# Kernel tuning notes

Measured on AMD Instinct MI355X. Metric: run time of the kernel, lower is better.

## Reference

```python
import jax, jax.numpy as jnp
import numpy as np

DIM = 192
STATE = 64
B = 8
H = 64
W = 64
EPS_LN = 1e-5
EPS_BN = 1e-5


def _layernorm(x, g, b):
    m = jnp.mean(x, axis=-1, keepdims=True)
    v = jnp.mean((x - m) ** 2, axis=-1, keepdims=True)
    return (x - m) / jnp.sqrt(v + EPS_LN) * g + b


def _linear(x, w, b=None):
    # torch Linear convention: w is [out, in]
    y = jnp.einsum('...i,oi->...o', x, w)
    return y if b is None else y + b


def _parallel_scan(A, Bd, xp):
    # A, Bd, xp: [B, L, S]; h_t = A_t*h_{t-1} + Bd_t*xp_t via log-space cumsum
    A_safe = jnp.clip(A, 0.001, 0.999)
    log_A = jnp.log(A_safe + 1e-10)
    log_cum_A = jnp.cumsum(log_A, axis=1)
    log_cum_A_max = jnp.max(log_cum_A, axis=1, keepdims=True)
    cum_A = jnp.exp(log_cum_A - log_cum_A_max)
    BX = Bd * xp
    # prepend zeros, drop last: normalizer uses cumprod up to t-1
    log_pad = jnp.pad(log_cum_A - log_cum_A_max, ((0, 0), (1, 0), (0, 0)))[:, :-1]
    BX_norm = BX * jnp.exp(-log_pad)
    return jnp.cumsum(BX_norm, axis=1) * cum_A


def _ssm(x, ln_g, ln_b, xp_w, xp_b, dt_w, dt_b, A_log, B_w, C_w, Dp, out_w, out_b):
    xn = _layernorm(x, ln_g, ln_b)
    delta = jax.nn.softplus(_linear(xn, dt_w, dt_b)) * 0.01 + 0.0001  # [B,L,S]
    B_t = _linear(xn, B_w)
    C_t = _linear(xn, C_w)
    A = -jnp.exp(A_log)  # [S]
    x_proj = _linear(xn, xp_w, xp_b)
    deltaA = jnp.clip(delta * A, -10.0, -0.0001)
    A_disc = jnp.exp(deltaA)
    B_disc = delta * B_t
    h = _parallel_scan(A_disc, B_disc, x_proj)
    y = C_t * h
    y = jnp.where(jnp.all(jnp.isfinite(y)), y, jnp.zeros_like(y))
    y = _linear(y, out_w, out_b)
    return y + jnp.clip(Dp, -2.0, 2.0) * x


def reference(x, ln1_g, ln1_b, ln2_g, ln2_b, dw_w, bn_g, bn_b, bn_rm, bn_rv,
              ssm_ln_g, ssm_ln_b, xp_w, xp_b, dt_w, dt_b, A_log, B_w, C_w,
              D_param, out_w, out_b, mlp_w1, mlp_b1, mlp_w2, mlp_b2,
              alpha_local, alpha_ssm, alpha_mlp):
    identity = x
    # depthwise 3x3 conv + BatchNorm2d (eval mode, running stats)
    xc = jax.lax.conv_general_dilated(
        x, dw_w, (1, 1), 'SAME', feature_group_count=DIM,
        dimension_numbers=('NCHW', 'OIHW', 'NCHW'))
    scale = (bn_g / jnp.sqrt(bn_rv + EPS_BN))[None, :, None, None]
    x_local = (xc - bn_rm[None, :, None, None]) * scale + bn_b[None, :, None, None]
    # SSM branch on flattened spatial sequence
    x_seq = x.transpose(0, 2, 3, 1).reshape(B, H * W, DIM)
    x_seq = _layernorm(x_seq, ln1_g, ln1_b)
    x_seq = _ssm(x_seq, ssm_ln_g, ssm_ln_b, xp_w, xp_b, dt_w, dt_b, A_log,
                 B_w, C_w, D_param, out_w, out_b)
    x_ssm = x_seq.reshape(B, H, W, DIM).transpose(0, 3, 1, 2)
    xr = identity + alpha_local * x_local + alpha_ssm * x_ssm
    # residual MLP (dropout = identity at inference)
    x_mlp = xr.transpose(0, 2, 3, 1).reshape(B, H * W, DIM)
    x_mlp = _layernorm(x_mlp, ln2_g, ln2_b)
    x_mlp = _linear(jax.nn.gelu(_linear(x_mlp, mlp_w1, mlp_b1), approximate=False),
                    mlp_w2, mlp_b2)
    return xr + alpha_mlp * x_mlp.reshape(B, H, W, DIM).transpose(0, 3, 1, 2)


def setup_inputs() -> dict:
    key = jax.random.key(0)
    ks = jax.random.split(key, 12)
    def nrm(k, shape, s):
        return jax.random.normal(k, shape, jnp.float32) * s
    f32 = jnp.float32
    return {
        'x': jax.random.normal(ks[0], (B, DIM, H, W), f32),
        'ln1_g': jnp.ones(DIM, f32), 'ln1_b': jnp.zeros(DIM, f32),
        'ln2_g': jnp.ones(DIM, f32), 'ln2_b': jnp.zeros(DIM, f32),
        'dw_w': nrm(ks[1], (DIM, 1, 3, 3), 0.2),
        'bn_g': jnp.ones(DIM, f32), 'bn_b': jnp.zeros(DIM, f32),
        'bn_rm': jnp.zeros(DIM, f32), 'bn_rv': jnp.ones(DIM, f32),
        'ssm_ln_g': jnp.ones(DIM, f32), 'ssm_ln_b': jnp.zeros(DIM, f32),
        'xp_w': nrm(ks[2], (STATE, DIM), 0.05), 'xp_b': jnp.zeros(STATE, f32),
        'dt_w': nrm(ks[3], (STATE, DIM), 0.05), 'dt_b': jnp.zeros(STATE, f32),
        'A_log': jnp.log(jax.random.uniform(ks[4], (STATE,), f32) * 0.8 + 0.2),
        'B_w': nrm(ks[5], (STATE, DIM), 0.05),
        'C_w': nrm(ks[6], (STATE, DIM), 0.05),
        'D_param': jnp.zeros(DIM, f32),
        'out_w': nrm(ks[7], (DIM, STATE), 0.05), 'out_b': jnp.zeros(DIM, f32),
        'mlp_w1': nrm(ks[8], (4 * DIM, DIM), 0.03), 'mlp_b1': jnp.zeros(4 * DIM, f32),
        'mlp_w2': nrm(ks[9], (DIM, 4 * DIM), 0.03), 'mlp_b2': jnp.zeros(DIM, f32),
        'alpha_local': jnp.full((1,), 0.5, f32),
        'alpha_ssm': jnp.full((1,), 0.5, f32),
        'alpha_mlp': jnp.full((1,), 0.5, f32),
    }
```

## Files before the change

kernel.cpp:

```cpp
#include <hip/hip_runtime.h>
#include <hip/hip_bf16.h>
#include <math.h>


#define DEV static __device__ __forceinline__

constexpr int Bn = 8, Dm = 192, Ln = 4096, Sn = 64, Hd = 768;

typedef __attribute__((ext_vector_type(8))) short bf16x8;
typedef __attribute__((ext_vector_type(4))) float f32x4;

DEV short f2b(float x) {
  __hip_bfloat16 h = __float2bfloat16(x);
  return *(short*)&h;
}

DEV float b2f(short x) {
  __hip_bfloat16 h = *(__hip_bfloat16*)&x;
  return __bfloat162float(h);
}

__global__ __launch_bounds__(256) void k_prep(
    const float* __restrict__ x, const float* __restrict__ g1, const float* __restrict__ b1,
    const float* __restrict__ g2, const float* __restrict__ b2,
    short* __restrict__ xnb, short* __restrict__ xln1b,
    const float* __restrict__ dt_w, const float* __restrict__ B_w,
    const float* __restrict__ C_w, const float* __restrict__ xp_w,
    const float* __restrict__ out_w, const float* __restrict__ w1,
    const float* __restrict__ w2, short* __restrict__ wb) {
  __shared__ __align__(16) float tile[Dm * 65];
  int tid = threadIdx.x;
  if (blockIdx.y == 8) {
    for (int i = blockIdx.x * 256 + tid; i < 89088; i += 64 * 256) {
      const float4* src;
      if (i < 3072)       src = (const float4*)dt_w + i;
      else if (i < 6144)  src = (const float4*)B_w + (i - 3072);
      else if (i < 9216)  src = (const float4*)C_w + (i - 6144);
      else if (i < 12288) src = (const float4*)xp_w + (i - 9216);
      else if (i < 15360) src = (const float4*)out_w + (i - 12288);
      else if (i < 52224) src = (const float4*)w1 + (i - 15360);
      else                src = (const float4*)w2 + (i - 52224);
      float4 v = *src;
      int o = i * 4;
      wb[o] = f2b(v.x); wb[o + 1] = f2b(v.y); wb[o + 2] = f2b(v.z); wb[o + 3] = f2b(v.w);
    }
    return;
  }
  int b = blockIdx.y, l0 = blockIdx.x * 64;
  const float* xb = x + (size_t)b * Dm * Ln;
  for (int i = tid; i < Dm * 16; i += 256) {
    int d = i >> 4, l4 = (i & 15) << 2;
    float4 v = *(const float4*)&xb[d * Ln + l0 + l4];
    tile[d * 65 + l4]     = v.x; tile[d * 65 + l4 + 1] = v.y;
    tile[d * 65 + l4 + 2] = v.z; tile[d * 65 + l4 + 3] = v.w;
  }
  __syncthreads();
  int pix = tid >> 2, part = tid & 3, c0 = part * 48;
  float v[48];
  float s1 = 0.f, q1 = 0.f;
#pragma unroll
  for (int j = 0; j < 48; j++) {
    float t = tile[(c0 + j) * 65 + pix];
    v[j] = t; s1 += t; q1 += t * t;
  }
  s1 += __shfl_xor(s1, 1); s1 += __shfl_xor(s1, 2);
  q1 += __shfl_xor(q1, 1); q1 += __shfl_xor(q1, 2);
  float m = s1 * (1.f / 192.f);
  float inv = rsqrtf(q1 * (1.f / 192.f) - m * m + 1e-5f);
  float s2 = 0.f, q2 = 0.f;
#pragma unroll
  for (int j = 0; j < 48; j++) {
    float y = (v[j] - m) * inv * g1[c0 + j] + b1[c0 + j];
    v[j] = y; s2 += y; q2 += y * y;
  }
  s2 += __shfl_xor(s2, 1); s2 += __shfl_xor(s2, 2);
  q2 += __shfl_xor(q2, 1); q2 += __shfl_xor(q2, 2);
  float m2 = s2 * (1.f / 192.f);
  float inv2 = rsqrtf(q2 * (1.f / 192.f) - m2 * m2 + 1e-5f);
  size_t base = ((size_t)b * Ln + l0 + pix) * Dm + c0;
#pragma unroll
  for (int j = 0; j < 48; j += 8) {
    int4 yo, no;
    short* yp = (short*)&yo; short* np = (short*)&no;
#pragma unroll
    for (int k = 0; k < 8; k++) {
      float y = v[j + k];
      yp[k] = f2b(y);
      np[k] = f2b((y - m2) * inv2 * g2[c0 + j + k] + b2[c0 + j + k]);
    }
    *(int4*)&xln1b[base + j] = yo;
    *(int4*)&xnb[base + j]   = no;
  }
}

__global__ __launch_bounds__(256) void k_projconv(
    const short* __restrict__ xnb, const short* __restrict__ wcat,
    const float* __restrict__ dt_b, const float* __restrict__ xp_b,
    const float* __restrict__ A_log, float* __restrict__ aA, unsigned* __restrict__ bxc,
    float* __restrict__ sums,
    const float* __restrict__ x, const float* __restrict__ dw,
    const float* __restrict__ bn_g, const float* __restrict__ bn_b,
    const float* __restrict__ bn_rm, const float* __restrict__ bn_rv,
    const float* __restrict__ a_loc, float* __restrict__ xr) {
  __shared__ __align__(16) short smem[64 * 72 + 256 * 72];
  int tid = threadIdx.x;
  if (blockIdx.x >= 512) {
    float* xs = (float*)smem;
    int i6 = blockIdx.x - 512;
    int d = i6 % 192, b = i6 / 192;
    const float* xp = x + ((size_t)b * Dm + d) * Ln;
    for (int i = tid; i < 1024; i += 256) ((float4*)xs)[i] = ((const float4*)xp)[i];
    __syncthreads();
    float w[9];
#pragma unroll
    for (int k = 0; k < 9; k++) w[k] = dw[d * 9 + k];
    float scale = bn_g[d] * rsqrtf(bn_rv[d] + 1e-5f);
    float rm = bn_rm[d], bb = bn_b[d];
    float al = a_loc[0];
    float* xo = xr + ((size_t)b * Dm + d) * Ln;
    for (int i = tid; i < 4096; i += 256) {
      int h = i >> 6, wc = i & 63;
      float acc = 0.f;
#pragma unroll
      for (int kh = 0; kh < 3; kh++) {
        int hh = h + kh - 1;
        if (hh < 0 || hh >= 64) continue;
#pragma unroll
        for (int kw = 0; kw < 3; kw++) {
          int ww2 = wc + kw - 1;
          if (ww2 < 0 || ww2 >= 64) continue;
          acc += xs[hh * 64 + ww2] * w[kh * 3 + kw];
        }
      }
      float xl = (acc - rm) * scale + bb;
      xo[i] = xs[i] + al * xl;
    }
    return;
  }
  short* As = smem;
  short* Bs = smem + 64 * 72;
  int m0 = blockIdx.x * 64;
  int lane = tid & 63, l16 = lane & 15, quad = lane >> 4, w = tid >> 6;
  f32x4 acc[16] = {};
  for (int kt = 0; kt < 3; kt++) {
    int kb = kt * 64;
    for (int i = tid; i < 512; i += 256) {
      int row = i >> 3, c8 = (i & 7) * 8;
      *(float4*)&As[row * 72 + c8] = *(const float4*)&xnb[(size_t)(m0 + row) * 192 + kb + c8];
    }
    for (int i = tid; i < 2048; i += 256) {
      int row = i >> 3, c8 = (i & 7) * 8;
      *(float4*)&Bs[row * 72 + c8] = *(const float4*)&wcat[(size_t)row * 192 + kb + c8];
    }
    __syncthreads();
#pragma unroll
    for (int ks = 0; ks < 2; ks++) {
      int ko = ks * 32 + quad * 8;
      bf16x8 a0 = *(const bf16x8*)&As[(w * 16 + l16) * 72 + ko];
#pragma unroll
      for (int nh = 0; nh < 2; nh++) {
        bf16x8 bfr[8];
#pragma unroll
        for (int j = 0; j < 8; j++) bfr[j] = *(const bf16x8*)&Bs[((nh * 8 + j) * 16 + l16) * 72 + ko];
#pragma unroll
        for (int j = 0; j < 8; j++)
          acc[nh * 8 + j] = __builtin_amdgcn_mfma_f32_16x16x32_bf16(a0, bfr[j], acc[nh * 8 + j], 0, 0, 0);
      }
    }
    __syncthreads();
  }
  float* aAs = (float*)Bs;
  float* bxs = aAs + 64 * 65;
  float Av[4], dtbv[4], xpbv[4];
#pragma unroll
  for (int ni = 0; ni < 4; ni++) {
    int s = ni * 16 + l16;
    Av[ni] = -expf(A_log[s]); dtbv[ni] = dt_b[s]; xpbv[ni] = xp_b[s];
  }
#pragma unroll
  for (int r = 0; r < 4; r++) {
    int lm = w * 16 + quad * 4 + r;
    int m = m0 + lm;
#pragma unroll
    for (int ni = 0; ni < 4; ni++) {
      int s = ni * 16 + l16;
      float z = acc[ni][r] + dtbv[ni];
      float sp = (z > 20.f) ? z : log1pf(expf(z));
      float delta = sp * 0.01f + 0.0001f;
      float bt  = acc[ni + 4][r];
      float ct  = acc[ni + 8][r];
      float xpv = acc[ni + 12][r] + xpbv[ni];
      float dA = fminf(fmaxf(delta * Av[ni], -10.f), -0.0001f);
      float Ae = fminf(fmaxf(expf(dA), 0.001f), 0.999f) + 1e-10f;
      short bxh = f2b(delta * bt * xpv);
      aA[(size_t)m * 64 + s] = Ae;
      unsigned pk = (unsigned)(unsigned short)bxh
                  | ((unsigned)(unsigned short)f2b(ct) << 16);
      bxc[(size_t)m * 64 + s] = pk;
      aAs[lm * 65 + s] = Ae;
      bxs[lm * 65 + s] = b2f(bxh);
    }
  }
  __syncthreads();
  int s = tid & 63, seg = tid >> 6, chunk = seg >> 1, sub = seg & 1;
  bool first = ((m0 & 4095) == 0) && (chunk == 0) && (sub == 0);
  float P = 1.f, H = 0.f;
  int base = chunk * 32 + sub * 16;
#pragma unroll
  for (int j = 0; j < 16; j++) {
    float a  = aAs[(base + j) * 65 + s];
    float bx = bxs[(base + j) * 65 + s];
    if (first && j == 0) { P = a; H = bx; }
    else { P *= a; H = a * (H + bx); }
  }
  float* partP = (float*)As;
  float* partH = partP + 256;
  partP[seg * 64 + s] = P; partH[seg * 64 + s] = H;
  __syncthreads();
  if (tid < 128) {
    int c = tid >> 6;
    float p0 = partP[(c * 2) * 64 + s], p1 = partP[(c * 2 + 1) * 64 + s];
    float h0 = partH[(c * 2) * 64 + s], h1 = partH[(c * 2 + 1) * 64 + s];
    int ci = (m0 >> 12) * 128 + ((m0 & 4095) >> 5) + c;
    sums[(ci * 2 + 0) * 64 + s] = p0 * p1;
    sums[(ci * 2 + 1) * 64 + s] = p1 * h0 + h1;
  }
}

__global__ __launch_bounds__(256) void k_out(
    const float* __restrict__ aA, const unsigned* __restrict__ bxc,
    const float* __restrict__ sums,
    const short* __restrict__ owb, const float* __restrict__ out_b,
    const float* __restrict__ Dp, const short* __restrict__ xln1b,
    const float* __restrict__ a_ssm, const float* __restrict__ g2,
    const float* __restrict__ bb2,
    float* __restrict__ xr, short* __restrict__ xn2) {
  __shared__ __align__(16) float smemf[64 * 193];
  short* As = (short*)smemf;
  short* Bs = (short*)smemf + 192 * 72;
  float* Pp   = smemf + 9216;
  float* Hp   = Pp + 256;
  float* cbuf = Hp + 256;
  float* tile = smemf;
  int l0g = blockIdx.x * 64, tid = threadIdx.x;
  int lane = tid & 63, l16 = lane & 15, quad = lane >> 4, wv = tid >> 6;
  for (int i = tid; i < 1536; i += 256) {
    int row = i >> 3, c8 = (i & 7) * 8;
    *(float4*)&As[row * 72 + c8] = *(const float4*)&owb[row * 64 + c8];
  }
  int bb = l0g >> 12, c0 = (l0g & 4095) >> 5;
  float xrv[3][4][4];
#pragma unroll
  for (int mi = 0; mi < 3; mi++)
#pragma unroll
    for (int r = 0; r < 4; r++) {
      int d = wv * 48 + mi * 16 + quad * 4 + r;
#pragma unroll
      for (int ni = 0; ni < 4; ni++) {
        int l = l0g + ni * 16 + l16;
        xrv[mi][r][ni] = xr[((size_t)bb * Dm + d) * Ln + (l & 4095)];
      }
    }
  int qstar = c0 >> 5, jstar = c0 & 31;
  float Pj0 = 1.f, Hj0 = 0.f, Pj1 = 1.f, Hj1 = 0.f;
  {
    int q = wv, s = lane;
    if (q <= qstar) {
      float P = 1.f, H = 0.f;
      int nj = (q == qstar) ? (jstar + 2) : 32;
      for (int j = 0; j < nj; j++) {
        if (q == qstar && j == jstar)     { Pj0 = P; Hj0 = H; }
        if (q == qstar && j == jstar + 1) { Pj1 = P; Hj1 = H; }
        int ci = bb * 128 + q * 32 + j;
        float a = sums[(ci * 2 + 0) * 64 + s];
        float h = sums[(ci * 2 + 1) * 64 + s];
        P *= a; H = a * H + h;
      }
      if (q < qstar) { Pp[q * 64 + s] = P; Hp[q * 64 + s] = H; }
    }
  }
  __syncthreads();
  if (wv == qstar) {
    float C = 0.f;
    for (int qq = 0; qq < qstar; qq++) C = Pp[qq * 64 + lane] * C + Hp[qq * 64 + lane];
    cbuf[lane]      = Pj0 * C + Hj0;
    cbuf[64 + lane] = Pj1 * C + Hj1;
  }
  __syncthreads();
  if (wv < 2) {
    int c = c0 + wv, s = lane;
    float h = cbuf[wv * 64 + s];
    const float* ap = aA + (size_t)(l0g + wv * 32) * 64;
    const unsigned* bp = bxc + (size_t)(l0g + wv * 32) * 64;
    int t = 0;
    if (c == 0) {
      unsigned u = bp[s];
      h = b2f((short)(u & 0xFFFF));
      Bs[(wv * 32) * 72 + s] = f2b(b2f((short)(u >> 16)) * h);
      t = 1;
    }
#pragma unroll 4
    for (; t < 32; t++) {
      unsigned u = bp[t * 64 + s];
      float a = ap[t * 64 + s];
      h = a * (h + b2f((short)(u & 0xFFFF)));
      Bs[(wv * 32 + t) * 72 + s] = f2b(b2f((short)(u >> 16)) * h);
    }
  }
  __syncthreads();
  f32x4 acc[3][4] = {};
#pragma unroll
  for (int ks = 0; ks < 2; ks++) {
    int ko = ks * 32 + quad * 8;
    bf16x8 a[3], b[4];
#pragma unroll
    for (int mi = 0; mi < 3; mi++) a[mi] = *(const bf16x8*)&As[(wv * 48 + mi * 16 + l16) * 72 + ko];
#pragma unroll
    for (int ni = 0; ni < 4; ni++) b[ni] = *(const bf16x8*)&Bs[(ni * 16 + l16) * 72 + ko];
#pragma unroll
    for (int mi = 0; mi < 3; mi++)
#pragma unroll
      for (int ni = 0; ni < 4; ni++)
        acc[mi][ni] = __builtin_amdgcn_mfma_f32_16x16x32_bf16(a[mi], b[ni], acc[mi][ni], 0, 0, 0);
  }
  __syncthreads();
  float as_ = a_ssm[0];
#pragma unroll
  for (int mi = 0; mi < 3; mi++)
#pragma unroll
    for (int r = 0; r < 4; r++) {
      int d = wv * 48 + mi * 16 + quad * 4 + r;
      float ob = out_b[d];
      float dc = fminf(fmaxf(Dp[d], -2.f), 2.f);
#pragma unroll
      for (int ni = 0; ni < 4; ni++) {
        int l = l0g + ni * 16 + l16;
        float v = acc[mi][ni][r] + ob;
        if (dc != 0.f) v += dc * b2f(xln1b[(size_t)l * 192 + d]);
        size_t idx = ((size_t)bb * Dm + d) * Ln + (l & 4095);
        float nx = xrv[mi][r][ni] + as_ * v;
        xr[idx] = nx;
        tile[(l & 63) * 193 + d] = nx;
      }
    }
  __syncthreads();
  int pix = tid >> 2, part = tid & 3, c0p = part * 48;
  float vv[48];
  float s1 = 0.f, q1 = 0.f;
#pragma unroll
  for (int j = 0; j < 48; j++) {
    float t = tile[pix * 193 + c0p + j];
    vv[j] = t; s1 += t; q1 += t * t;
  }
  s1 += __shfl_xor(s1, 1); s1 += __shfl_xor(s1, 2);
  q1 += __shfl_xor(q1, 1); q1 += __shfl_xor(q1, 2);
  float m = s1 * (1.f / 192.f);
  float inv = rsqrtf(q1 * (1.f / 192.f) - m * m + 1e-5f);
  size_t obase = (size_t)(l0g + pix) * Dm + c0p;
#pragma unroll
  for (int j = 0; j < 48; j += 8) {
    int4 no; short* np = (short*)&no;
#pragma unroll
    for (int k = 0; k < 8; k++)
      np[k] = f2b((vv[j + k] - m) * inv * g2[c0p + j + k] + bb2[c0p + j + k]);
    *(int4*)&xn2[obase + j] = no;
  }
}

__global__ __launch_bounds__(256) void k_gemm1(
    const short* __restrict__ xn2, const short* __restrict__ w1b,
    const float* __restrict__ b1h, short* __restrict__ hid) {
  __shared__ __align__(16) short smem[128 * 72 + 64 * 72];
  short* As = smem;
  short* Bs = smem + 128 * 72;
  int bid = blockIdx.x;
  int xcd = bid & 7, p = bid >> 3;
  int m0 = (xcd * 32 + p / 12) * 128, n0 = (p % 12) * 64;
  int tid = threadIdx.x;
  int lane = tid & 63, l16 = lane & 15, quad = lane >> 4;
  int wm = (tid >> 6) >> 1, wn = (tid >> 6) & 1;
  f32x4 acc[4][2] = {};
  for (int kt = 0; kt < 3; kt++) {
    int kb = kt * 64;
    for (int i = tid; i < 1024; i += 256) {
      int row = i >> 3, c8 = (i & 7) * 8;
      *(float4*)&As[row * 72 + c8] = *(const float4*)&xn2[(size_t)(m0 + row) * 192 + kb + c8];
    }
    for (int i = tid; i < 512; i += 256) {
      int row = i >> 3, c8 = (i & 7) * 8;
      *(float4*)&Bs[row * 72 + c8] = *(const float4*)&w1b[(size_t)(n0 + row) * 192 + kb + c8];
    }
    __syncthreads();
#pragma unroll
    for (int ks = 0; ks < 2; ks++) {
      int ko = ks * 32 + quad * 8;
      bf16x8 a[4], b[2];
#pragma unroll
      for (int mi = 0; mi < 4; mi++) a[mi] = *(const bf16x8*)&As[(wm * 64 + mi * 16 + l16) * 72 + ko];
#pragma unroll
      for (int ni = 0; ni < 2; ni++) b[ni] = *(const bf16x8*)&Bs[(wn * 32 + ni * 16 + l16) * 72 + ko];
#pragma unroll
      for (int mi = 0; mi < 4; mi++)
#pragma unroll
        for (int ni = 0; ni < 2; ni++)
          acc[mi][ni] = __builtin_amdgcn_mfma_f32_16x16x32_bf16(a[mi], b[ni], acc[mi][ni], 0, 0, 0);
    }
    __syncthreads();
  }
  short* Cs = smem;
  float bias2[2];
#pragma unroll
  for (int ni = 0; ni < 2; ni++) bias2[ni] = b1h[n0 + wn * 32 + ni * 16 + l16];
#pragma unroll
  for (int mi = 0; mi < 4; mi++)
#pragma unroll
    for (int ni = 0; ni < 2; ni++) {
      int n = wn * 32 + ni * 16 + l16;
#pragma unroll
      for (int r = 0; r < 4; r++) {
        int m = wm * 64 + mi * 16 + quad * 4 + r;
        float v = acc[mi][ni][r] + bias2[ni];
        float g = 0.5f * v * (1.f + erff(v * 0.70710678118f));
        Cs[m * 72 + n] = f2b(g);
      }
    }
  __syncthreads();
  for (int i = tid; i < 1024; i += 256) {
    int m = i >> 3, ch = i & 7;
    *(float4*)&hid[(size_t)(m0 + m) * 768 + n0 + ch * 8] = *(const float4*)&Cs[m * 72 + ch * 8];
  }
}

__global__ __launch_bounds__(256) void k_gemm2(
    const short* __restrict__ hid, const short* __restrict__ w2b,
    const float* __restrict__ b2o, const float* __restrict__ xr,
    const float* __restrict__ am, float* __restrict__ out) {
  __shared__ __align__(16) short Wt[96 * 72];
  __shared__ __align__(16) short Ht[64 * 72];
  int bid = blockIdx.x;
  int xcd = bid & 7, p = bid >> 3;
  int l0g = (xcd * 64 + (p >> 1)) * 64, d0 = (p & 1) * 96;
  int tid = threadIdx.x;
  int lane = tid & 63, l16 = lane & 15, quad = lane >> 4;
  int wm = (tid >> 6) >> 1, wn = (tid >> 6) & 1;
  f32x4 acc[3][2] = {};
  for (int kt = 0; kt < 12; kt++) {
    int kb = kt * 64;
    for (int i = tid; i < 768; i += 256) {
      int row = i >> 3, c8 = (i & 7) * 8;
      *(float4*)&Wt[row * 72 + c8] = *(const float4*)&w2b[(size_t)(d0 + row) * 768 + kb + c8];
    }
    for (int i = tid; i < 512; i += 256) {
      int row = i >> 3, c8 = (i & 7) * 8;
      *(float4*)&Ht[row * 72 + c8] = *(const float4*)&hid[(size_t)(l0g + row) * 768 + kb + c8];
    }
    __syncthreads();
#pragma unroll
    for (int ks = 0; ks < 2; ks++) {
      int ko = ks * 32 + quad * 8;
      bf16x8 a[3], b[2];
#pragma unroll
      for (int mi = 0; mi < 3; mi++) a[mi] = *(const bf16x8*)&Wt[(wm * 48 + mi * 16 + l16) * 72 + ko];
#pragma unroll
      for (int ni = 0; ni < 2; ni++) b[ni] = *(const bf16x8*)&Ht[(wn * 32 + ni * 16 + l16) * 72 + ko];
#pragma unroll
      for (int mi = 0; mi < 3; mi++)
#pragma unroll
        for (int ni = 0; ni < 2; ni++)
          acc[mi][ni] = __builtin_amdgcn_mfma_f32_16x16x32_bf16(a[mi], b[ni], acc[mi][ni], 0, 0, 0);
    }
    __syncthreads();
  }
  float alpha = am[0];
#pragma unroll
  for (int mi = 0; mi < 3; mi++)
#pragma unroll
    for (int r = 0; r < 4; r++) {
      int d = d0 + wm * 48 + mi * 16 + quad * 4 + r;
      float bias = b2o[d];
#pragma unroll
      for (int ni = 0; ni < 2; ni++) {
        int lg = l0g + wn * 32 + ni * 16 + l16;
        size_t idx = ((size_t)(lg >> 12) * Dm + d) * Ln + (lg & 4095);
        out[idx] = xr[idx] + alpha * (acc[mi][ni][r] + bias);
      }
    }
}

extern "C" void kernel_launch(void* const* d_in, const int* in_sizes, int n_in,
                              void* d_out, int out_size, void* d_ws, size_t ws_size,
                              hipStream_t stream) {
  (void)in_sizes; (void)n_in; (void)out_size; (void)ws_size;
  const float* x     = (const float*)d_in[0];
  const float* ln1_g = (const float*)d_in[1];
  const float* ln1_b = (const float*)d_in[2];
  const float* ln2_g = (const float*)d_in[3];
  const float* ln2_b = (const float*)d_in[4];
  const float* dw_w  = (const float*)d_in[5];
  const float* bn_g  = (const float*)d_in[6];
  const float* bn_b  = (const float*)d_in[7];
  const float* bn_rm = (const float*)d_in[8];
  const float* bn_rv = (const float*)d_in[9];
  const float* ssm_g = (const float*)d_in[10];
  const float* ssm_b = (const float*)d_in[11];
  const float* xp_w  = (const float*)d_in[12];
  const float* xp_b  = (const float*)d_in[13];
  const float* dt_w  = (const float*)d_in[14];
  const float* dt_b  = (const float*)d_in[15];
  const float* A_log = (const float*)d_in[16];
  const float* B_w   = (const float*)d_in[17];
  const float* C_w   = (const float*)d_in[18];
  const float* Dp    = (const float*)d_in[19];
  const float* out_w = (const float*)d_in[20];
  const float* out_b = (const float*)d_in[21];
  const float* w1    = (const float*)d_in[22];
  const float* b1    = (const float*)d_in[23];
  const float* w2    = (const float*)d_in[24];
  const float* b2    = (const float*)d_in[25];
  const float* a_loc = (const float*)d_in[26];
  const float* a_ssm = (const float*)d_in[27];
  const float* a_mlp = (const float*)d_in[28];

  float* ws = (float*)d_ws;
  short*    xnb   = (short*)ws;
  short*    xln1b = (short*)(ws + 3145728);
  float*    aA    = ws + 6291456;
  unsigned* bxc   = (unsigned*)(ws + 8388608);
  float*    xr    = ws + 17825792;
  short*    wb    = (short*)(ws + 24117248);
  float*    sums  = ws + 24829952;
  short*    xn2   = (short*)(ws + 25026560);
  short*    hid   = (short*)(ws + 28172288);
  short*    wcatb = wb;
  short*    owb   = wb + 49152;
  short*    w1b   = wb + 61440;
  short*    w2b   = wb + 208896;
  float*    out   = (float*)d_out;

  k_prep    <<<dim3(64, 9), 256, 0, stream>>>(x, ln1_g, ln1_b, ssm_g, ssm_b, xnb, xln1b,
                                              dt_w, B_w, C_w, xp_w, out_w, w1, w2, wb);
  k_projconv<<<dim3(2048),  256, 0, stream>>>(xnb, wcatb, dt_b, xp_b, A_log, aA, bxc, sums,
                                              x, dw_w, bn_g, bn_b, bn_rm, bn_rv, a_loc, xr);
  k_out     <<<dim3(512),   256, 0, stream>>>(aA, bxc, sums, owb, out_b, Dp, xln1b,
                                              a_ssm, ln2_g, ln2_b, xr, xn2);
  k_gemm1   <<<dim3(3072),  256, 0, stream>>>(xn2, w1b, b1, hid);
  k_gemm2   <<<dim3(1024),  256, 0, stream>>>(hid, w2b, b2, xr, a_mlp, out);
}
```

Measured before the change: 278.1 us.

## Split conv out of projection kernel and use tanh-approximate GELU

Separates the depthwise conv + BN path from the projection GEMM kernel into its own launch, so the GEMM blocks get dedicated LDS sizing without the branch. Also replaces erf-based GELU in gemm1 epilogue with the tanh approximation using __expf. The split adds a kernel launch and removes overlap between conv and GEMM blocks; the tanh GELU changes numerics slightly and is an approximation of the reference's exact GELU.

```diff
diff --git a/kernel.cpp b/kernel.cpp
--- a/kernel.cpp
+++ b/kernel.cpp
@@ -93,53 +93,14 @@
   }
 }
 
-__global__ __launch_bounds__(256) void k_projconv(
+__global__ __launch_bounds__(256) void k_proj(
     const short* __restrict__ xnb, const short* __restrict__ wcat,
     const float* __restrict__ dt_b, const float* __restrict__ xp_b,
     const float* __restrict__ A_log, float* __restrict__ aA, unsigned* __restrict__ bxc,
-    float* __restrict__ sums,
-    const float* __restrict__ x, const float* __restrict__ dw,
-    const float* __restrict__ bn_g, const float* __restrict__ bn_b,
-    const float* __restrict__ bn_rm, const float* __restrict__ bn_rv,
-    const float* __restrict__ a_loc, float* __restrict__ xr) {
-  __shared__ __align__(16) short smem[64 * 72 + 256 * 72];
-  int tid = threadIdx.x;
-  if (blockIdx.x >= 512) {
-    float* xs = (float*)smem;
-    int i6 = blockIdx.x - 512;
-    int d = i6 % 192, b = i6 / 192;
-    const float* xp = x + ((size_t)b * Dm + d) * Ln;
-    for (int i = tid; i < 1024; i += 256) ((float4*)xs)[i] = ((const float4*)xp)[i];
-    __syncthreads();
-    float w[9];
-#pragma unroll
-    for (int k = 0; k < 9; k++) w[k] = dw[d * 9 + k];
-    float scale = bn_g[d] * rsqrtf(bn_rv[d] + 1e-5f);
-    float rm = bn_rm[d], bb = bn_b[d];
-    float al = a_loc[0];
-    float* xo = xr + ((size_t)b * Dm + d) * Ln;
-    for (int i = tid; i < 4096; i += 256) {
-      int h = i >> 6, wc = i & 63;
-      float acc = 0.f;
-#pragma unroll
-      for (int kh = 0; kh < 3; kh++) {
-        int hh = h + kh - 1;
-        if (hh < 0 || hh >= 64) continue;
-#pragma unroll
-        for (int kw = 0; kw < 3; kw++) {
-          int ww2 = wc + kw - 1;
-          if (ww2 < 0 || ww2 >= 64) continue;
-          acc += xs[hh * 64 + ww2] * w[kh * 3 + kw];
-        }
-      }
-      float xl = (acc - rm) * scale + bb;
-      xo[i] = xs[i] + al * xl;
-    }
-    return;
-  }
-  short* As = smem;
-  short* Bs = smem + 64 * 72;
-  int m0 = blockIdx.x * 64;
+    float* __restrict__ sums) {
+  __shared__ __align__(16) short As[64 * 72];
+  __shared__ __align__(16) short Bs[256 * 72];
+  int m0 = blockIdx.x * 64, tid = threadIdx.x;
   int lane = tid & 63, l16 = lane & 15, quad = lane >> 4, w = tid >> 6;
   f32x4 acc[16] = {};
   for (int kt = 0; kt < 3; kt++) {
@@ -224,6 +185,42 @@
     int ci = (m0 >> 12) * 128 + ((m0 & 4095) >> 5) + c;
     sums[(ci * 2 + 0) * 64 + s] = p0 * p1;
     sums[(ci * 2 + 1) * 64 + s] = p1 * h0 + h1;
+  }
+}
+
+__global__ __launch_bounds__(256) void k_conv(
+    const float* __restrict__ x, const float* __restrict__ dw,
+    const float* __restrict__ bn_g, const float* __restrict__ bn_b,
+    const float* __restrict__ bn_rm, const float* __restrict__ bn_rv,
+    const float* __restrict__ a_loc, float* __restrict__ xr) {
+  __shared__ __align__(16) float xs[64 * 64];
+  int d = blockIdx.x, b = blockIdx.y, tid = threadIdx.x;
+  const float* xp = x + ((size_t)b * Dm + d) * Ln;
+  for (int i = tid; i < 1024; i += 256) ((float4*)xs)[i] = ((const float4*)xp)[i];
+  __syncthreads();
+  float w[9];
+#pragma unroll
+  for (int k = 0; k < 9; k++) w[k] = dw[d * 9 + k];
+  float scale = bn_g[d] * rsqrtf(bn_rv[d] + 1e-5f);
+  float rm = bn_rm[d], bb = bn_b[d];
+  float al = a_loc[0];
+  float* xo = xr + ((size_t)b * Dm + d) * Ln;
+  for (int i = tid; i < 4096; i += 256) {
+    int h = i >> 6, wc = i & 63;
+    float acc = 0.f;
+#pragma unroll
+    for (int kh = 0; kh < 3; kh++) {
+      int hh = h + kh - 1;
+      if (hh < 0 || hh >= 64) continue;
+#pragma unroll
+      for (int kw = 0; kw < 3; kw++) {
+        int ww2 = wc + kw - 1;
+        if (ww2 < 0 || ww2 >= 64) continue;
+        acc += xs[hh * 64 + ww2] * w[kh * 3 + kw];
+      }
+    }
+    float xl = (acc - rm) * scale + bb;
+    xo[i] = xs[i] + al * xl;
   }
 }
 
@@ -420,7 +417,9 @@
       for (int r = 0; r < 4; r++) {
         int m = wm * 64 + mi * 16 + quad * 4 + r;
         float v = acc[mi][ni][r] + bias2[ni];
-        float g = 0.5f * v * (1.f + erff(v * 0.70710678118f));
+        float u = 0.7978845608f * (v + 0.044715f * v * v * v);
+        float e = __expf(2.f * u);
+        float g = 0.5f * v * (1.f + (e - 1.f) / (e + 1.f));
         Cs[m * 72 + n] = f2b(g);
       }
     }
@@ -537,12 +536,12 @@
   short*    w2b   = wb + 208896;
   float*    out   = (float*)d_out;
 
-  k_prep    <<<dim3(64, 9), 256, 0, stream>>>(x, ln1_g, ln1_b, ssm_g, ssm_b, xnb, xln1b,
-                                              dt_w, B_w, C_w, xp_w, out_w, w1, w2, wb);
-  k_projconv<<<dim3(2048),  256, 0, stream>>>(xnb, wcatb, dt_b, xp_b, A_log, aA, bxc, sums,
-                                              x, dw_w, bn_g, bn_b, bn_rm, bn_rv, a_loc, xr);
-  k_out     <<<dim3(512),   256, 0, stream>>>(aA, bxc, sums, owb, out_b, Dp, xln1b,
-                                              a_ssm, ln2_g, ln2_b, xr, xn2);
-  k_gemm1   <<<dim3(3072),  256, 0, stream>>>(xn2, w1b, b1, hid);
-  k_gemm2   <<<dim3(1024),  256, 0, stream>>>(hid, w2b, b2, xr, a_mlp, out);
-}
+  k_prep <<<dim3(64, 9),  256, 0, stream>>>(x, ln1_g, ln1_b, ssm_g, ssm_b, xnb, xln1b,
+                                            dt_w, B_w, C_w, xp_w, out_w, w1, w2, wb);
+  k_proj <<<dim3(512),    256, 0, stream>>>(xnb, wcatb, dt_b, xp_b, A_log, aA, bxc, sums);
+  k_conv <<<dim3(192, 8), 256, 0, stream>>>(x, dw_w, bn_g, bn_b, bn_rm, bn_rv, a_loc, xr);
+  k_out  <<<dim3(512),    256, 0, stream>>>(aA, bxc, sums, owb, out_b, Dp, xln1b,
+                                            a_ssm, ln2_g, ln2_b, xr, xn2);
+  k_gemm1<<<dim3(3072),   256, 0, stream>>>(xn2, w1b, b1, hid);
+  k_gemm2<<<dim3(1024),   256, 0, stream>>>(hid, w2b, b2, xr, a_mlp, out);
+}
```

Result: faster. 268.9 us (-3.3%).
